# Performance work log

Measured on AMD Instinct MI355X. Metric: run time of the kernel, lower is better.

Reference implementation:

```python
import jax, jax.numpy as jnp
import numpy as np

BN_EPS = 1e-5

def setup_inputs() -> dict:
    key = jax.random.key(0)
    ks = jax.random.split(key, 8)
    B, C, O, M, K, NR, NT = 64, 8, 8, 32, 32, 8, 8
    ini = float(np.sqrt(3.0 / O / C))
    def p(k):
        return jax.random.uniform(k, (O, C), jnp.float32, -ini, ini)
    return {
        "A": jax.random.normal(ks[0], (B, C, M, K, NR, NT), jnp.float32),
        "P1": p(ks[1]), "P2": p(ks[2]), "P3": p(ks[3]), "P4": p(ks[4]), "P5": p(ks[5]),
        "Wq": p(ks[6]), "Wk": p(ks[7]),
        "gamma": jnp.ones((O,), jnp.float32),
        "beta": jnp.zeros((O,), jnp.float32),
    }

def reference(A, P1, P2, P3, P4, P5, Wq, Wk, gamma, beta):
    B, C, M, Kd, NR, NT = A.shape
    # Branch 1: per-element channel mix, full tensor
    A1 = jnp.einsum('oc,bcmkrt->bomkrt', P1, A)                    # [B,O,M,K,NR,NT]
    # Branch 2: mean over M (axis 2)
    A2 = jnp.einsum('oc,bckrt->bokrt', P2, A.mean(2))[:, :, None]  # [B,O,1,K,NR,NT]
    # Branch 3: mean over NT (axis 5)
    A3 = jnp.einsum('oc,bcmkr->bomkr', P3, A.mean(5))[..., None]   # [B,O,M,K,NR,1]
    # Branch 4: mean over NR (axis 4)
    A4 = jnp.einsum('oc,bcmkt->bomkt', P4, A.mean(4))[:, :, :, :, None, :]  # [B,O,M,K,1,NT]
    # Attention branch over the K axis, built from mean over NR
    temp = A.mean(4)                                               # [B,C,M,K,NT]
    q = jnp.einsum('oc,bcmkt->bomkt', Wq, temp)
    k = jnp.einsum('oc,bcmkt->bomkt', Wk, temp)
    v = jnp.einsum('oc,bcmkt->bomkt', P5, temp)
    alpha = jnp.tanh(jnp.einsum('bomkt,bomlt->bomkl', q, k) / NT)  # [B,O,M,K,K]
    A5 = (jnp.einsum('bomkl,bomlt->bomkt', alpha, v) / Kd)[:, :, :, :, None, :]
    out = A1 + 0.1 * A2 + 0.1 * A3 + 0.5 * A4 + 2.0 * A5          # [B,O,M,K,NR,NT]
    out = jax.nn.relu(out)
    # BatchNorm1d (training mode, biased var) over all dims except channel O
    mean = out.mean(axis=(0, 2, 3, 4, 5), keepdims=True)
    var = out.var(axis=(0, 2, 3, 4, 5), keepdims=True)
    g = gamma[None, :, None, None, None, None]
    bta = beta[None, :, None, None, None, None]
    return (out - mean) * jax.lax.rsqrt(var + BN_EPS) * g + bta
```

## Files before the change

kernel.cpp:

```cpp
#include <hip/hip_runtime.h>
#include <hip/hip_fp16.h>


using u16 = unsigned short;
using u32 = unsigned int;
typedef float f32x4 __attribute__((ext_vector_type(4)));

#define NTOT 33554432u
#define PLANE 65536u

__device__ __forceinline__ void ld8f(const float* p, float* f) {
  float4 a = *(const float4*)p;
  float4 b = *(const float4*)(p + 4);
  f[0] = a.x; f[1] = a.y; f[2] = a.z; f[3] = a.w;
  f[4] = b.x; f[5] = b.y; f[6] = b.z; f[7] = b.w;
}
__device__ __forceinline__ void st8f(float* p, const float* f) {
  *(float4*)p = make_float4(f[0], f[1], f[2], f[3]);
  *(float4*)(p + 4) = make_float4(f[4], f[5], f[6], f[7]);
}
__device__ __forceinline__ void st8f_nt(float* p, const float* f) {
  f32x4 a = {f[0], f[1], f[2], f[3]};
  f32x4 b = {f[4], f[5], f[6], f[7]};
  __builtin_nontemporal_store(a, (f32x4*)p);
  __builtin_nontemporal_store(b, (f32x4*)(p + 4));
}
__device__ __forceinline__ u16 f2h(float f) {
  __half h = __float2half_rn(f);
  return *(u16*)&h;
}
__device__ __forceinline__ float h2f(u16 x) {
  __half h = *(__half*)&x;
  return __half2float(h);
}
__device__ __forceinline__ float fast_tanh(float x) {
  float e = __expf(2.0f * x);
  return 1.0f - 2.0f / (e + 1.0f);
}

__global__ __launch_bounds__(1024) void k1a_mmean(
    const float* __restrict__ A, float* __restrict__ mcab,
    float* __restrict__ stats) {
  __shared__ float red[4][256][9];
  const int b = blockIdx.x >> 3;
  const int c = blockIdx.x & 7;
  const int tid = threadIdx.x;
  if (blockIdx.x == 0 && tid < 16) stats[tid] = 0.0f;
  const int mh = tid >> 8;
  const int jt = tid & 255;
  const float* base = A + (size_t)(b * 8 + c) * 65536 + (size_t)mh * 8 * 2048 + jt * 8;
  float acc[8];
#pragma unroll
  for (int t = 0; t < 8; ++t) acc[t] = 0.0f;
#pragma unroll
  for (int m = 0; m < 8; ++m) {
    float ar[8];
    ld8f(base + m * 2048, ar);
#pragma unroll
    for (int t = 0; t < 8; ++t) acc[t] += ar[t];
  }
#pragma unroll
  for (int t = 0; t < 8; ++t) red[mh][jt][t] = acc[t];
  __syncthreads();
  if (mh == 0) {
    float s[8];
#pragma unroll
    for (int t = 0; t < 8; ++t)
      s[t] = (red[0][jt][t] + red[1][jt][t] + red[2][jt][t] + red[3][jt][t]) *
             (1.0f / 32.0f);
    st8f(mcab + (size_t)(b * 8 + c) * 2048 + jt * 8, s);
  }
}

__global__ void k1b_p2(float* __restrict__ mcab, const float* __restrict__ P2) {
  const int b = blockIdx.x >> 3;
  const int j = (blockIdx.x & 7) * 256 + threadIdx.x;
  float mc[8];
#pragma unroll
  for (int c = 0; c < 8; ++c) mc[c] = mcab[(size_t)(b * 8 + c) * 2048 + j];
  float a2[8];
#pragma unroll
  for (int o = 0; o < 8; ++o) {
    float s = 0.0f;
#pragma unroll
    for (int c = 0; c < 8; ++c) s = fmaf(P2[o * 8 + c], mc[c], s);
    a2[o] = 0.1f * s;
  }
#pragma unroll
  for (int o = 0; o < 8; ++o) mcab[(size_t)(b * 8 + o) * 2048 + j] = a2[o];
}

template <int MODE>
__global__ __launch_bounds__(256, 2) void k2_main(
    const float* __restrict__ A,
    const float* __restrict__ a2pre,
    const float* __restrict__ P1,
    const float* __restrict__ P3,
    const float* __restrict__ P4,
    const float* __restrict__ P5,
    const float* __restrict__ Wq,
    const float* __restrict__ Wk,
    float* __restrict__ outp,
    u16* __restrict__ xb,
    float* __restrict__ stats,
    const u32 rsplit) {
  __shared__ float qb[8 * 260];
  __shared__ float kb[8 * 260];
  __shared__ float vb[8 * 260];
  __shared__ float a5b[8 * 260];
  __shared__ float sred[64];

  const int tid = threadIdx.x;
  const int b = blockIdx.x >> 5;
  const int m = blockIdx.x & 31;
  const int k = tid >> 3;
  const int r = tid & 7;

  float acc[8][8];
  float acc3[8];
  float qv[8], kv[8], vv[8];
#pragma unroll
  for (int o = 0; o < 8; ++o) {
    acc3[o] = 0.0f;
#pragma unroll
    for (int t = 0; t < 8; ++t) acc[o][t] = 0.0f;
  }
#pragma unroll
  for (int t = 0; t < 8; ++t) { qv[t] = 0.0f; kv[t] = 0.0f; vv[t] = 0.0f; }

#pragma unroll
  for (int c = 0; c < 8; ++c) {
    float ar[8];
    ld8f(A + ((size_t)((b * 8 + c) * 32 + m) * 2048 + tid * 8), ar);
    float trc[8];
#pragma unroll
    for (int t = 0; t < 8; ++t) {
      float x = ar[t];
      x += __shfl_xor(x, 1, 64);
      x += __shfl_xor(x, 2, 64);
      x += __shfl_xor(x, 4, 64);
      trc[t] = x * 0.125f;
    }
    const float mtc = (ar[0] + ar[1] + ar[2] + ar[3] +
                       ar[4] + ar[5] + ar[6] + ar[7]) * 0.125f;
#pragma unroll
    for (int o = 0; o < 8; ++o) {
      const float w1 = P1[o * 8 + c];
      const float w4 = 0.5f * P4[o * 8 + c];
      acc3[o] = fmaf(0.1f * P3[o * 8 + c], mtc, acc3[o]);
#pragma unroll
      for (int t = 0; t < 8; ++t)
        acc[o][t] = fmaf(w1, ar[t], fmaf(w4, trc[t], acc[o][t]));
    }
    const float wq = Wq[r * 8 + c];
    const float wk = Wk[r * 8 + c];
    const float wv = P5[r * 8 + c];
#pragma unroll
    for (int t = 0; t < 8; ++t) {
      qv[t] = fmaf(wq, trc[t], qv[t]);
      kv[t] = fmaf(wk, trc[t], kv[t]);
      vv[t] = fmaf(wv, trc[t], vv[t]);
    }
  }

#pragma unroll
  for (int o = 0; o < 8; ++o) {
    float a2v[8];
    ld8f(a2pre + ((size_t)(b * 8 + o) * 2048 + tid * 8), a2v);
#pragma unroll
    for (int t = 0; t < 8; ++t) acc[o][t] += a2v[t] + acc3[o];
  }

  st8f(&qb[r * 260 + k * 8], qv);
  st8f(&kb[r * 260 + k * 8], kv);
  st8f(&vb[r * 260 + k * 8], vv);
  __syncthreads();

  {
    const int o = tid >> 5;
    const int kq = (tid >> 2) & 7;
    const int lo = tid & 3;
    float qf[4][8];
#pragma unroll
    for (int kl = 0; kl < 4; ++kl)
      ld8f(&qb[o * 260 + (kq * 4 + kl) * 8], qf[kl]);
    float a5p[4][8];
#pragma unroll
    for (int kl = 0; kl < 4; ++kl)
#pragma unroll
      for (int t = 0; t < 8; ++t) a5p[kl][t] = 0.0f;

#pragma unroll
    for (int ll = 0; ll < 8; ++ll) {
      const int l = lo * 8 + ll;
      float krw[8];
      ld8f(&kb[o * 260 + l * 8], krw);
      float al[4];
#pragma unroll
      for (int kl = 0; kl < 4; ++kl) {
        float s = 0.0f;
#pragma unroll
        for (int t = 0; t < 8; ++t) s = fmaf(qf[kl][t], krw[t], s);
        al[kl] = fast_tanh(s * 0.125f);
      }
      float vrw[8];
      ld8f(&vb[o * 260 + l * 8], vrw);
#pragma unroll
      for (int kl = 0; kl < 4; ++kl)
#pragma unroll
        for (int t = 0; t < 8; ++t)
          a5p[kl][t] = fmaf(al[kl], vrw[t], a5p[kl][t]);
    }
#pragma unroll
    for (int kl = 0; kl < 4; ++kl)
#pragma unroll
      for (int t = 0; t < 8; ++t) {
        float x = a5p[kl][t];
        x += __shfl_xor(x, 1, 64);
        x += __shfl_xor(x, 2, 64);
        a5p[kl][t] = x * 0.0625f;
      }
#pragma unroll
    for (int kl = 0; kl < 4; ++kl) {
      const float w0 = lo == 0 ? a5p[kl][0] : lo == 1 ? a5p[kl][2]
                      : lo == 2 ? a5p[kl][4] : a5p[kl][6];
      const float w1 = lo == 0 ? a5p[kl][1] : lo == 1 ? a5p[kl][3]
                      : lo == 2 ? a5p[kl][5] : a5p[kl][7];
      *(float2*)&a5b[o * 260 + (kq * 4 + kl) * 8 + lo * 2] = make_float2(w0, w1);
    }
  }
  __syncthreads();

  float psum[8], psq[8];
#pragma unroll
  for (int o = 0; o < 8; ++o) { psum[o] = 0.0f; psq[o] = 0.0f; }
  const size_t outbase = (size_t)(b * 256 + m) * 2048 + tid * 8;
#pragma unroll
  for (int o = 0; o < 8; ++o) {
    float a5f[8];
    ld8f(&a5b[o * 260 + k * 8], a5f);
    float x8[8];
#pragma unroll
    for (int t = 0; t < 8; ++t) {
      float x = acc[o][t] + a5f[t];
      x = fmaxf(x, 0.0f);
      psum[o] += x;
      psq[o] = fmaf(x, x, psq[o]);
      x8[t] = x;
    }
    const size_t idx = outbase + (size_t)o * 65536;
    if (MODE == 0) {
      st8f(outp + idx, x8);
    } else {
      uint4 u;
      u.x = (u32)f2h(x8[0]) | ((u32)f2h(x8[1]) << 16);
      u.y = (u32)f2h(x8[2]) | ((u32)f2h(x8[3]) << 16);
      u.z = (u32)f2h(x8[4]) | ((u32)f2h(x8[5]) << 16);
      u.w = (u32)f2h(x8[6]) | ((u32)f2h(x8[7]) << 16);
      u16* dst;
      if (MODE == 1) {
        dst = xb;
      } else {
        dst = (idx >= (size_t)rsplit) ? (u16*)outp : xb;
      }
      *(uint4*)(dst + idx) = u;
    }
  }
#pragma unroll
  for (int o = 0; o < 8; ++o) {
    float s = psum[o], q = psq[o];
#pragma unroll
    for (int mask = 32; mask >= 1; mask >>= 1) {
      s += __shfl_xor(s, mask, 64);
      q += __shfl_xor(q, mask, 64);
    }
    psum[o] = s; psq[o] = q;
  }
  const int lane = tid & 63;
  const int wid = tid >> 6;
  if (lane == 0) {
#pragma unroll
    for (int o = 0; o < 8; ++o) {
      sred[wid * 16 + o * 2] = psum[o];
      sred[wid * 16 + o * 2 + 1] = psq[o];
    }
  }
  __syncthreads();
  if (tid < 16) {
    float s = sred[tid] + sred[16 + tid] + sred[32 + tid] + sred[48 + tid];
    atomicAdd(&stats[tid], s);
  }
}

__global__ void k3_fp16(const u16* __restrict__ src, float* __restrict__ outp,
                        const float* __restrict__ stats,
                        const float* __restrict__ gamma,
                        const float* __restrict__ beta,
                        const u32 ebase) {
  const size_t e0 = (size_t)ebase + ((size_t)blockIdx.x * 256 + threadIdx.x) * 8;
  const int o = (int)(e0 >> 16) & 7;
  const float inv_n = 1.0f / 4194304.0f;
  const float mean = stats[o * 2] * inv_n;
  float var = stats[o * 2 + 1] * inv_n - mean * mean;
  var = fmaxf(var, 0.0f);
  const float inv = rsqrtf(var + 1e-5f);
  const float g = gamma[o] * inv;
  const float sh = beta[o] - mean * g;
  const uint4 u = *(const uint4*)(src + e0);
  float f[8];
  f[0] = h2f((u16)(u.x & 0xffffu)); f[1] = h2f((u16)(u.x >> 16));
  f[2] = h2f((u16)(u.y & 0xffffu)); f[3] = h2f((u16)(u.y >> 16));
  f[4] = h2f((u16)(u.z & 0xffffu)); f[5] = h2f((u16)(u.z >> 16));
  f[6] = h2f((u16)(u.w & 0xffffu)); f[7] = h2f((u16)(u.w >> 16));
#pragma unroll
  for (int t = 0; t < 8; ++t) f[t] = fmaf(f[t], g, sh);
  st8f_nt(outp + e0, f);
}

__global__ void k3_norm_inplace(float* __restrict__ outp,
                                const float* __restrict__ stats,
                                const float* __restrict__ gamma,
                                const float* __restrict__ beta) {
  const int idx = blockIdx.x * 256 + threadIdx.x;
  const size_t e0 = (size_t)idx * 8;
  const int o = (int)(e0 >> 16) & 7;
  const float inv_n = 1.0f / 4194304.0f;
  const float mean = stats[o * 2] * inv_n;
  float var = stats[o * 2 + 1] * inv_n - mean * mean;
  var = fmaxf(var, 0.0f);
  const float inv = rsqrtf(var + 1e-5f);
  const float g = gamma[o] * inv;
  const float sh = beta[o] - mean * g;
  float f[8];
  ld8f(outp + e0, f);
#pragma unroll
  for (int t = 0; t < 8; ++t) f[t] = fmaf(f[t], g, sh);
  st8f_nt(outp + e0, f);
}

extern "C" void kernel_launch(void* const* d_in, const int* in_sizes, int n_in,
                              void* d_out, int out_size, void* d_ws, size_t ws_size,
                              hipStream_t stream) {
  const float* A  = (const float*)d_in[0];
  const float* P1 = (const float*)d_in[1];
  const float* P2 = (const float*)d_in[2];
  const float* P3 = (const float*)d_in[3];
  const float* P4 = (const float*)d_in[4];
  const float* P5 = (const float*)d_in[5];
  const float* Wq = (const float*)d_in[6];
  const float* Wk = (const float*)d_in[7];
  const float* gamma = (const float*)d_in[8];
  const float* beta  = (const float*)d_in[9];
  float* outp = (float*)d_out;

  float* stats = (float*)d_ws;
  float* mcab = (float*)((char*)d_ws + 256);
  u16* xb = (u16*)((char*)d_ws + 256 + (size_t)4 * 1024 * 1024);
  const size_t UWB = 256 + (size_t)4 * 1024 * 1024;
  const size_t need_full = UWB + (size_t)2 * NTOT;

  hipLaunchKernelGGL(k1a_mmean, dim3(512), dim3(1024), 0, stream, A, mcab, stats);
  hipLaunchKernelGGL(k1b_p2, dim3(512), dim3(256), 0, stream, mcab, P2);

  if (ws_size >= need_full) {
    hipLaunchKernelGGL((k2_main<1>), dim3(2048), dim3(256), 0, stream,
                       A, mcab, P1, P3, P4, P5, Wq, Wk, outp, xb, stats, 0u);
    hipLaunchKernelGGL(k3_fp16, dim3(16384), dim3(256), 0, stream,
                       xb, outp, stats, gamma, beta, 0u);
  } else {
    const size_t avail = (ws_size > UWB) ? (ws_size - UWB) : 0;
    u32 R = NTOT / 2;
    while (R > PLANE && (size_t)2 * R > avail) R >>= 1;
    if ((size_t)2 * R <= avail) {
      hipLaunchKernelGGL((k2_main<2>), dim3(2048), dim3(256), 0, stream,
                         A, mcab, P1, P3, P4, P5, Wq, Wk, outp, xb, stats, R);
      for (u32 S = NTOT / 2; S >= R; S >>= 1) {
        hipLaunchKernelGGL(k3_fp16, dim3(S / 2048), dim3(256), 0, stream,
                           (const u16*)outp, outp, stats, gamma, beta, S);
      }
      hipLaunchKernelGGL(k3_fp16, dim3(R / 2048), dim3(256), 0, stream,
                         xb, outp, stats, gamma, beta, 0u);
    } else {
      hipLaunchKernelGGL((k2_main<0>), dim3(2048), dim3(256), 0, stream,
                         A, mcab, P1, P3, P4, P5, Wq, Wk, outp, xb, stats, 0u);
      hipLaunchKernelGGL(k3_norm_inplace, dim3(16384), dim3(256), 0, stream,
                         outp, stats, gamma, beta);
    }
  }
}
```

Measured before the change: 387.3 us.

## Fuse main pass and batchnorm apply via cooperative grid sync with register staging

Replaces the two-pass main kernel plus fp16 workspace normalize kernel with a single cooperative kernel of 512 blocks. Each block processes four m slices, keeps the ReLU outputs packed as fp16 in registers, grid-syncs once the BN statistics are accumulated, then normalizes and writes fp32 output directly. This removes the fp16 intermediate write and read-back through global memory and one kernel launch. In exchange it adds heavy register pressure from the 128-register staging array, a grid-wide barrier, and a fallback path if cooperative launch fails.

```diff
diff --git a/kernel.cpp b/kernel.cpp
--- a/kernel.cpp
+++ b/kernel.cpp
@@ -1,13 +1,13 @@
 #include <hip/hip_runtime.h>
 #include <hip/hip_fp16.h>
+#include <hip/hip_cooperative_groups.h>
+
+namespace cg = cooperative_groups;
 
 
 using u16 = unsigned short;
 using u32 = unsigned int;
 typedef float f32x4 __attribute__((ext_vector_type(4)));
-
-#define NTOT 33554432u
-#define PLANE 65536u
 
 __device__ __forceinline__ void ld8f(const float* p, float* f) {
   float4 a = *(const float4*)p;
@@ -90,7 +90,236 @@
   for (int o = 0; o < 8; ++o) mcab[(size_t)(b * 8 + o) * 2048 + j] = a2[o];
 }
 
-template <int MODE>
+__global__ __launch_bounds__(256, 2) void k2_fused(
+    const float* __restrict__ A,
+    const float* __restrict__ a2pre,
+    const float* __restrict__ P1,
+    const float* __restrict__ P3,
+    const float* __restrict__ P4,
+    const float* __restrict__ P5,
+    const float* __restrict__ Wq,
+    const float* __restrict__ Wk,
+    const float* __restrict__ gamma,
+    const float* __restrict__ beta,
+    float* __restrict__ outp,
+    float* __restrict__ stats) {
+  __shared__ float qb[8 * 260];
+  __shared__ float kb[8 * 260];
+  __shared__ float vb[8 * 260];
+  __shared__ float a5b[8 * 260];
+  __shared__ float sred[64];
+
+  const int tid = threadIdx.x;
+  const int b = blockIdx.x >> 3;
+  const int mg = blockIdx.x & 7;
+  const int k = tid >> 3;
+  const int r = tid & 7;
+
+  u32 stg[4][8][4];
+  float psum[8], psq[8];
+#pragma unroll
+  for (int o = 0; o < 8; ++o) { psum[o] = 0.0f; psq[o] = 0.0f; }
+
+#pragma unroll
+  for (int mi = 0; mi < 4; ++mi) {
+    const int m = mg * 4 + mi;
+
+    float acc[8][8];
+    float acc3[8];
+    float qv[8], kv[8], vv[8];
+#pragma unroll
+    for (int o = 0; o < 8; ++o) {
+      acc3[o] = 0.0f;
+#pragma unroll
+      for (int t = 0; t < 8; ++t) acc[o][t] = 0.0f;
+    }
+#pragma unroll
+    for (int t = 0; t < 8; ++t) { qv[t] = 0.0f; kv[t] = 0.0f; vv[t] = 0.0f; }
+
+#pragma unroll
+    for (int c = 0; c < 8; ++c) {
+      float ar[8];
+      ld8f(A + ((size_t)((b * 8 + c) * 32 + m) * 2048 + tid * 8), ar);
+      float trc[8];
+#pragma unroll
+      for (int t = 0; t < 8; ++t) {
+        float x = ar[t];
+        x += __shfl_xor(x, 1, 64);
+        x += __shfl_xor(x, 2, 64);
+        x += __shfl_xor(x, 4, 64);
+        trc[t] = x * 0.125f;
+      }
+      const float mtc = (ar[0] + ar[1] + ar[2] + ar[3] +
+                         ar[4] + ar[5] + ar[6] + ar[7]) * 0.125f;
+#pragma unroll
+      for (int o = 0; o < 8; ++o) {
+        const float w1 = P1[o * 8 + c];
+        const float w4 = 0.5f * P4[o * 8 + c];
+        acc3[o] = fmaf(0.1f * P3[o * 8 + c], mtc, acc3[o]);
+#pragma unroll
+        for (int t = 0; t < 8; ++t)
+          acc[o][t] = fmaf(w1, ar[t], fmaf(w4, trc[t], acc[o][t]));
+      }
+      const float wq = Wq[r * 8 + c];
+      const float wk = Wk[r * 8 + c];
+      const float wv = P5[r * 8 + c];
+#pragma unroll
+      for (int t = 0; t < 8; ++t) {
+        qv[t] = fmaf(wq, trc[t], qv[t]);
+        kv[t] = fmaf(wk, trc[t], kv[t]);
+        vv[t] = fmaf(wv, trc[t], vv[t]);
+      }
+    }
+
+#pragma unroll
+    for (int o = 0; o < 8; ++o) {
+      float a2v[8];
+      ld8f(a2pre + ((size_t)(b * 8 + o) * 2048 + tid * 8), a2v);
+#pragma unroll
+      for (int t = 0; t < 8; ++t) acc[o][t] += a2v[t] + acc3[o];
+    }
+
+    st8f(&qb[r * 260 + k * 8], qv);
+    st8f(&kb[r * 260 + k * 8], kv);
+    st8f(&vb[r * 260 + k * 8], vv);
+    __syncthreads();
+
+    {
+      const int o = tid >> 5;
+      const int kq = (tid >> 2) & 7;
+      const int lo = tid & 3;
+      float qf[4][8];
+#pragma unroll
+      for (int kl = 0; kl < 4; ++kl)
+        ld8f(&qb[o * 260 + (kq * 4 + kl) * 8], qf[kl]);
+      float a5p[4][8];
+#pragma unroll
+      for (int kl = 0; kl < 4; ++kl)
+#pragma unroll
+        for (int t = 0; t < 8; ++t) a5p[kl][t] = 0.0f;
+
+#pragma unroll
+      for (int ll = 0; ll < 8; ++ll) {
+        const int l = lo * 8 + ll;
+        float krw[8];
+        ld8f(&kb[o * 260 + l * 8], krw);
+        float al[4];
+#pragma unroll
+        for (int kl = 0; kl < 4; ++kl) {
+          float s = 0.0f;
+#pragma unroll
+          for (int t = 0; t < 8; ++t) s = fmaf(qf[kl][t], krw[t], s);
+          al[kl] = fast_tanh(s * 0.125f);
+        }
+        float vrw[8];
+        ld8f(&vb[o * 260 + l * 8], vrw);
+#pragma unroll
+        for (int kl = 0; kl < 4; ++kl)
+#pragma unroll
+          for (int t = 0; t < 8; ++t)
+            a5p[kl][t] = fmaf(al[kl], vrw[t], a5p[kl][t]);
+      }
+#pragma unroll
+      for (int kl = 0; kl < 4; ++kl)
+#pragma unroll
+        for (int t = 0; t < 8; ++t) {
+          float x = a5p[kl][t];
+          x += __shfl_xor(x, 1, 64);
+          x += __shfl_xor(x, 2, 64);
+          a5p[kl][t] = x * 0.0625f;
+        }
+#pragma unroll
+      for (int kl = 0; kl < 4; ++kl) {
+        const float w0 = lo == 0 ? a5p[kl][0] : lo == 1 ? a5p[kl][2]
+                        : lo == 2 ? a5p[kl][4] : a5p[kl][6];
+        const float w1 = lo == 0 ? a5p[kl][1] : lo == 1 ? a5p[kl][3]
+                        : lo == 2 ? a5p[kl][5] : a5p[kl][7];
+        *(float2*)&a5b[o * 260 + (kq * 4 + kl) * 8 + lo * 2] = make_float2(w0, w1);
+      }
+    }
+    __syncthreads();
+
+#pragma unroll
+    for (int o = 0; o < 8; ++o) {
+      float a5f[8];
+      ld8f(&a5b[o * 260 + k * 8], a5f);
+      float x8[8];
+#pragma unroll
+      for (int t = 0; t < 8; ++t) {
+        float x = acc[o][t] + a5f[t];
+        x = fmaxf(x, 0.0f);
+        psum[o] += x;
+        psq[o] = fmaf(x, x, psq[o]);
+        x8[t] = x;
+      }
+      stg[mi][o][0] = (u32)f2h(x8[0]) | ((u32)f2h(x8[1]) << 16);
+      stg[mi][o][1] = (u32)f2h(x8[2]) | ((u32)f2h(x8[3]) << 16);
+      stg[mi][o][2] = (u32)f2h(x8[4]) | ((u32)f2h(x8[5]) << 16);
+      stg[mi][o][3] = (u32)f2h(x8[6]) | ((u32)f2h(x8[7]) << 16);
+    }
+  }
+
+#pragma unroll
+  for (int o = 0; o < 8; ++o) {
+    float s = psum[o], q = psq[o];
+#pragma unroll
+    for (int mask = 32; mask >= 1; mask >>= 1) {
+      s += __shfl_xor(s, mask, 64);
+      q += __shfl_xor(q, mask, 64);
+    }
+    psum[o] = s; psq[o] = q;
+  }
+  const int lane = tid & 63;
+  const int wid = tid >> 6;
+  if (lane == 0) {
+#pragma unroll
+    for (int o = 0; o < 8; ++o) {
+      sred[wid * 16 + o * 2] = psum[o];
+      sred[wid * 16 + o * 2 + 1] = psq[o];
+    }
+  }
+  __syncthreads();
+  if (tid < 16) {
+    float s = sred[tid] + sred[16 + tid] + sred[32 + tid] + sred[48 + tid];
+    atomicAdd(&stats[tid], s);
+  }
+
+  __threadfence();
+  cg::this_grid().sync();
+  __threadfence();
+
+  float gg[8], shh[8];
+#pragma unroll
+  for (int o = 0; o < 8; ++o) {
+    const float inv_n = 1.0f / 4194304.0f;
+    const float mean = stats[o * 2] * inv_n;
+    float var = stats[o * 2 + 1] * inv_n - mean * mean;
+    var = fmaxf(var, 0.0f);
+    const float inv = rsqrtf(var + 1e-5f);
+    gg[o] = gamma[o] * inv;
+    shh[o] = beta[o] - mean * gg[o];
+  }
+#pragma unroll
+  for (int mi = 0; mi < 4; ++mi) {
+    const int m = mg * 4 + mi;
+#pragma unroll
+    for (int o = 0; o < 8; ++o) {
+      float f[8];
+      f[0] = h2f((u16)(stg[mi][o][0] & 0xffffu));
+      f[1] = h2f((u16)(stg[mi][o][0] >> 16));
+      f[2] = h2f((u16)(stg[mi][o][1] & 0xffffu));
+      f[3] = h2f((u16)(stg[mi][o][1] >> 16));
+      f[4] = h2f((u16)(stg[mi][o][2] & 0xffffu));
+      f[5] = h2f((u16)(stg[mi][o][2] >> 16));
+      f[6] = h2f((u16)(stg[mi][o][3] & 0xffffu));
+      f[7] = h2f((u16)(stg[mi][o][3] >> 16));
+#pragma unroll
+      for (int t = 0; t < 8; ++t) f[t] = fmaf(f[t], gg[o], shh[o]);
+      st8f_nt(outp + ((size_t)((b * 8 + o) * 32 + m) * 2048 + tid * 8), f);
+    }
+  }
+}
+
 __global__ __launch_bounds__(256, 2) void k2_main(
     const float* __restrict__ A,
     const float* __restrict__ a2pre,
@@ -101,9 +330,7 @@
     const float* __restrict__ Wq,
     const float* __restrict__ Wk,
     float* __restrict__ outp,
-    u16* __restrict__ xb,
-    float* __restrict__ stats,
-    const u32 rsplit) {
+    float* __restrict__ stats) {
   __shared__ float qb[8 * 260];
   __shared__ float kb[8 * 260];
   __shared__ float vb[8 * 260];
@@ -248,23 +475,7 @@
       psq[o] = fmaf(x, x, psq[o]);
       x8[t] = x;
     }
-    const size_t idx = outbase + (size_t)o * 65536;
-    if (MODE == 0) {
-      st8f(outp + idx, x8);
-    } else {
-      uint4 u;
-      u.x = (u32)f2h(x8[0]) | ((u32)f2h(x8[1]) << 16);
-      u.y = (u32)f2h(x8[2]) | ((u32)f2h(x8[3]) << 16);
-      u.z = (u32)f2h(x8[4]) | ((u32)f2h(x8[5]) << 16);
-      u.w = (u32)f2h(x8[6]) | ((u32)f2h(x8[7]) << 16);
-      u16* dst;
-      if (MODE == 1) {
-        dst = xb;
-      } else {
-        dst = (idx >= (size_t)rsplit) ? (u16*)outp : xb;
-      }
-      *(uint4*)(dst + idx) = u;
-    }
+    st8f(outp + (outbase + (size_t)o * 65536), x8);
   }
 #pragma unroll
   for (int o = 0; o < 8; ++o) {
@@ -290,31 +501,6 @@
     float s = sred[tid] + sred[16 + tid] + sred[32 + tid] + sred[48 + tid];
     atomicAdd(&stats[tid], s);
   }
-}
-
-__global__ void k3_fp16(const u16* __restrict__ src, float* __restrict__ outp,
-                        const float* __restrict__ stats,
-                        const float* __restrict__ gamma,
-                        const float* __restrict__ beta,
-                        const u32 ebase) {
-  const size_t e0 = (size_t)ebase + ((size_t)blockIdx.x * 256 + threadIdx.x) * 8;
-  const int o = (int)(e0 >> 16) & 7;
-  const float inv_n = 1.0f / 4194304.0f;
-  const float mean = stats[o * 2] * inv_n;
-  float var = stats[o * 2 + 1] * inv_n - mean * mean;
-  var = fmaxf(var, 0.0f);
-  const float inv = rsqrtf(var + 1e-5f);
-  const float g = gamma[o] * inv;
-  const float sh = beta[o] - mean * g;
-  const uint4 u = *(const uint4*)(src + e0);
-  float f[8];
-  f[0] = h2f((u16)(u.x & 0xffffu)); f[1] = h2f((u16)(u.x >> 16));
-  f[2] = h2f((u16)(u.y & 0xffffu)); f[3] = h2f((u16)(u.y >> 16));
-  f[4] = h2f((u16)(u.z & 0xffffu)); f[5] = h2f((u16)(u.z >> 16));
-  f[6] = h2f((u16)(u.w & 0xffffu)); f[7] = h2f((u16)(u.w >> 16));
-#pragma unroll
-  for (int t = 0; t < 8; ++t) f[t] = fmaf(f[t], g, sh);
-  st8f_nt(outp + e0, f);
 }
 
 __global__ void k3_norm_inplace(float* __restrict__ outp,
@@ -355,36 +541,22 @@
 
   float* stats = (float*)d_ws;
   float* mcab = (float*)((char*)d_ws + 256);
-  u16* xb = (u16*)((char*)d_ws + 256 + (size_t)4 * 1024 * 1024);
-  const size_t UWB = 256 + (size_t)4 * 1024 * 1024;
-  const size_t need_full = UWB + (size_t)2 * NTOT;
 
   hipLaunchKernelGGL(k1a_mmean, dim3(512), dim3(1024), 0, stream, A, mcab, stats);
   hipLaunchKernelGGL(k1b_p2, dim3(512), dim3(256), 0, stream, mcab, P2);
 
-  if (ws_size >= need_full) {
-    hipLaunchKernelGGL((k2_main<1>), dim3(2048), dim3(256), 0, stream,
-                       A, mcab, P1, P3, P4, P5, Wq, Wk, outp, xb, stats, 0u);
-    hipLaunchKernelGGL(k3_fp16, dim3(16384), dim3(256), 0, stream,
-                       xb, outp, stats, gamma, beta, 0u);
-  } else {
-    const size_t avail = (ws_size > UWB) ? (ws_size - UWB) : 0;
-    u32 R = NTOT / 2;
-    while (R > PLANE && (size_t)2 * R > avail) R >>= 1;
-    if ((size_t)2 * R <= avail) {
-      hipLaunchKernelGGL((k2_main<2>), dim3(2048), dim3(256), 0, stream,
-                         A, mcab, P1, P3, P4, P5, Wq, Wk, outp, xb, stats, R);
-      for (u32 S = NTOT / 2; S >= R; S >>= 1) {
-        hipLaunchKernelGGL(k3_fp16, dim3(S / 2048), dim3(256), 0, stream,
-                           (const u16*)outp, outp, stats, gamma, beta, S);
-      }
-      hipLaunchKernelGGL(k3_fp16, dim3(R / 2048), dim3(256), 0, stream,
-                         xb, outp, stats, gamma, beta, 0u);
-    } else {
-      hipLaunchKernelGGL((k2_main<0>), dim3(2048), dim3(256), 0, stream,
-                         A, mcab, P1, P3, P4, P5, Wq, Wk, outp, xb, stats, 0u);
-      hipLaunchKernelGGL(k3_norm_inplace, dim3(16384), dim3(256), 0, stream,
-                         outp, stats, gamma, beta);
-    }
-  }
-}
+  void* kargs[] = {
+    (void*)&A, (void*)&mcab, (void*)&P1, (void*)&P3, (void*)&P4, (void*)&P5,
+    (void*)&Wq, (void*)&Wk, (void*)&gamma, (void*)&beta, (void*)&outp,
+    (void*)&stats
+  };
+  hipError_t err = hipLaunchCooperativeKernel(
+      (const void*)k2_fused, dim3(512), dim3(256), kargs, 0, stream);
+  if (err != hipSuccess) {
+    (void)hipGetLastError();
+    hipLaunchKernelGGL(k2_main, dim3(2048), dim3(256), 0, stream,
+                       A, mcab, P1, P3, P4, P5, Wq, Wk, outp, stats);
+    hipLaunchKernelGGL(k3_norm_inplace, dim3(16384), dim3(256), 0, stream,
+                       outp, stats, gamma, beta);
+  }
+}
```

Measured after the change: 711.0 us. +83.6%, slower.

## Stage fp16 intermediate in output buffer and expand it in place by slices

Applied to the files above, without the earlier changes.

The main kernel now always writes the fp16 pre-normalisation values into the first half of the output buffer, instead of into a separate workspace region. The lowest 1 MB of those values is copied aside into the workspace. A cascade of slice kernels then expands the upper halves to normalised fp32 in place, working from the top down, and the last slice reads from the saved copy. The q and a5 shared buffers are also merged to cut LDS use, at the cost of an extra barrier. The aim is to drop the large workspace buffer and keep fp16 data in the output lines. In exchange the schedule adds several serialised launches, the smaller of which underfill the GPU.

```diff
diff --git a/kernel.cpp b/kernel.cpp
--- a/kernel.cpp
+++ b/kernel.cpp
@@ -7,7 +7,6 @@
 typedef float f32x4 __attribute__((ext_vector_type(4)));
 
 #define NTOT 33554432u
-#define PLANE 65536u
 
 __device__ __forceinline__ void ld8f(const float* p, float* f) {
   float4 a = *(const float4*)p;
@@ -90,7 +89,6 @@
   for (int o = 0; o < 8; ++o) mcab[(size_t)(b * 8 + o) * 2048 + j] = a2[o];
 }
 
-template <int MODE>
 __global__ __launch_bounds__(256, 2) void k2_main(
     const float* __restrict__ A,
     const float* __restrict__ a2pre,
@@ -101,13 +99,10 @@
     const float* __restrict__ Wq,
     const float* __restrict__ Wk,
     float* __restrict__ outp,
-    u16* __restrict__ xb,
-    float* __restrict__ stats,
-    const u32 rsplit) {
-  __shared__ float qb[8 * 260];
+    float* __restrict__ stats) {
+  __shared__ float qa5[8 * 260];
   __shared__ float kb[8 * 260];
   __shared__ float vb[8 * 260];
-  __shared__ float a5b[8 * 260];
   __shared__ float sred[64];
 
   const int tid = threadIdx.x;
@@ -171,7 +166,7 @@
     for (int t = 0; t < 8; ++t) acc[o][t] += a2v[t] + acc3[o];
   }
 
-  st8f(&qb[r * 260 + k * 8], qv);
+  st8f(&qa5[r * 260 + k * 8], qv);
   st8f(&kb[r * 260 + k * 8], kv);
   st8f(&vb[r * 260 + k * 8], vv);
   __syncthreads();
@@ -183,7 +178,9 @@
     float qf[4][8];
 #pragma unroll
     for (int kl = 0; kl < 4; ++kl)
-      ld8f(&qb[o * 260 + (kq * 4 + kl) * 8], qf[kl]);
+      ld8f(&qa5[o * 260 + (kq * 4 + kl) * 8], qf[kl]);
+    __syncthreads();
+
     float a5p[4][8];
 #pragma unroll
     for (int kl = 0; kl < 4; ++kl)
@@ -226,7 +223,7 @@
                       : lo == 2 ? a5p[kl][4] : a5p[kl][6];
       const float w1 = lo == 0 ? a5p[kl][1] : lo == 1 ? a5p[kl][3]
                       : lo == 2 ? a5p[kl][5] : a5p[kl][7];
-      *(float2*)&a5b[o * 260 + (kq * 4 + kl) * 8 + lo * 2] = make_float2(w0, w1);
+      *(float2*)&qa5[o * 260 + (kq * 4 + kl) * 8 + lo * 2] = make_float2(w0, w1);
     }
   }
   __syncthreads();
@@ -234,11 +231,10 @@
   float psum[8], psq[8];
 #pragma unroll
   for (int o = 0; o < 8; ++o) { psum[o] = 0.0f; psq[o] = 0.0f; }
-  const size_t outbase = (size_t)(b * 256 + m) * 2048 + tid * 8;
 #pragma unroll
   for (int o = 0; o < 8; ++o) {
     float a5f[8];
-    ld8f(&a5b[o * 260 + k * 8], a5f);
+    ld8f(&qa5[o * 260 + k * 8], a5f);
     float x8[8];
 #pragma unroll
     for (int t = 0; t < 8; ++t) {
@@ -248,23 +244,13 @@
       psq[o] = fmaf(x, x, psq[o]);
       x8[t] = x;
     }
-    const size_t idx = outbase + (size_t)o * 65536;
-    if (MODE == 0) {
-      st8f(outp + idx, x8);
-    } else {
-      uint4 u;
-      u.x = (u32)f2h(x8[0]) | ((u32)f2h(x8[1]) << 16);
-      u.y = (u32)f2h(x8[2]) | ((u32)f2h(x8[3]) << 16);
-      u.z = (u32)f2h(x8[4]) | ((u32)f2h(x8[5]) << 16);
-      u.w = (u32)f2h(x8[6]) | ((u32)f2h(x8[7]) << 16);
-      u16* dst;
-      if (MODE == 1) {
-        dst = xb;
-      } else {
-        dst = (idx >= (size_t)rsplit) ? (u16*)outp : xb;
-      }
-      *(uint4*)(dst + idx) = u;
-    }
+    uint4 u;
+    u.x = (u32)f2h(x8[0]) | ((u32)f2h(x8[1]) << 16);
+    u.y = (u32)f2h(x8[2]) | ((u32)f2h(x8[3]) << 16);
+    u.z = (u32)f2h(x8[4]) | ((u32)f2h(x8[5]) << 16);
+    u.w = (u32)f2h(x8[6]) | ((u32)f2h(x8[7]) << 16);
+    const size_t e = (size_t)((b * 8 + o) * 32 + m) * 2048 + tid * 8;
+    *(uint4*)((char*)outp + 2 * e) = u;
   }
 #pragma unroll
   for (int o = 0; o < 8; ++o) {
@@ -292,11 +278,16 @@
   }
 }
 
-__global__ void k3_fp16(const u16* __restrict__ src, float* __restrict__ outp,
-                        const float* __restrict__ stats,
-                        const float* __restrict__ gamma,
-                        const float* __restrict__ beta,
-                        const u32 ebase) {
+__global__ void k3_copy(const uint4* __restrict__ src, uint4* __restrict__ dst) {
+  const int i = blockIdx.x * 256 + threadIdx.x;
+  dst[i] = src[i];
+}
+
+__global__ void k3_slice(const u16* __restrict__ src, float* __restrict__ outp,
+                         const float* __restrict__ stats,
+                         const float* __restrict__ gamma,
+                         const float* __restrict__ beta,
+                         const u32 ebase) {
   const size_t e0 = (size_t)ebase + ((size_t)blockIdx.x * 256 + threadIdx.x) * 8;
   const int o = (int)(e0 >> 16) & 7;
   const float inv_n = 1.0f / 4194304.0f;
@@ -317,27 +308,6 @@
   st8f_nt(outp + e0, f);
 }
 
-__global__ void k3_norm_inplace(float* __restrict__ outp,
-                                const float* __restrict__ stats,
-                                const float* __restrict__ gamma,
-                                const float* __restrict__ beta) {
-  const int idx = blockIdx.x * 256 + threadIdx.x;
-  const size_t e0 = (size_t)idx * 8;
-  const int o = (int)(e0 >> 16) & 7;
-  const float inv_n = 1.0f / 4194304.0f;
-  const float mean = stats[o * 2] * inv_n;
-  float var = stats[o * 2 + 1] * inv_n - mean * mean;
-  var = fmaxf(var, 0.0f);
-  const float inv = rsqrtf(var + 1e-5f);
-  const float g = gamma[o] * inv;
-  const float sh = beta[o] - mean * g;
-  float f[8];
-  ld8f(outp + e0, f);
-#pragma unroll
-  for (int t = 0; t < 8; ++t) f[t] = fmaf(f[t], g, sh);
-  st8f_nt(outp + e0, f);
-}
-
 extern "C" void kernel_launch(void* const* d_in, const int* in_sizes, int n_in,
                               void* d_out, int out_size, void* d_ws, size_t ws_size,
                               hipStream_t stream) {
@@ -355,36 +325,20 @@
 
   float* stats = (float*)d_ws;
   float* mcab = (float*)((char*)d_ws + 256);
-  u16* xb = (u16*)((char*)d_ws + 256 + (size_t)4 * 1024 * 1024);
-  const size_t UWB = 256 + (size_t)4 * 1024 * 1024;
-  const size_t need_full = UWB + (size_t)2 * NTOT;
 
   hipLaunchKernelGGL(k1a_mmean, dim3(512), dim3(1024), 0, stream, A, mcab, stats);
   hipLaunchKernelGGL(k1b_p2, dim3(512), dim3(256), 0, stream, mcab, P2);
-
-  if (ws_size >= need_full) {
-    hipLaunchKernelGGL((k2_main<1>), dim3(2048), dim3(256), 0, stream,
-                       A, mcab, P1, P3, P4, P5, Wq, Wk, outp, xb, stats, 0u);
-    hipLaunchKernelGGL(k3_fp16, dim3(16384), dim3(256), 0, stream,
-                       xb, outp, stats, gamma, beta, 0u);
-  } else {
-    const size_t avail = (ws_size > UWB) ? (ws_size - UWB) : 0;
-    u32 R = NTOT / 2;
-    while (R > PLANE && (size_t)2 * R > avail) R >>= 1;
-    if ((size_t)2 * R <= avail) {
-      hipLaunchKernelGGL((k2_main<2>), dim3(2048), dim3(256), 0, stream,
-                         A, mcab, P1, P3, P4, P5, Wq, Wk, outp, xb, stats, R);
-      for (u32 S = NTOT / 2; S >= R; S >>= 1) {
-        hipLaunchKernelGGL(k3_fp16, dim3(S / 2048), dim3(256), 0, stream,
-                           (const u16*)outp, outp, stats, gamma, beta, S);
-      }
-      hipLaunchKernelGGL(k3_fp16, dim3(R / 2048), dim3(256), 0, stream,
-                         xb, outp, stats, gamma, beta, 0u);
-    } else {
-      hipLaunchKernelGGL((k2_main<0>), dim3(2048), dim3(256), 0, stream,
-                         A, mcab, P1, P3, P4, P5, Wq, Wk, outp, xb, stats, 0u);
-      hipLaunchKernelGGL(k3_norm_inplace, dim3(16384), dim3(256), 0, stream,
-                         outp, stats, gamma, beta);
-    }
-  }
-}
+  hipLaunchKernelGGL(k2_main, dim3(2048), dim3(256), 0, stream,
+                     A, mcab, P1, P3, P4, P5, Wq, Wk, outp, stats);
+
+  hipLaunchKernelGGL(k3_copy, dim3(256), dim3(256), 0, stream,
+                     (const uint4*)outp, (uint4*)mcab);
+
+  const u16* s16 = (const u16*)outp;
+  for (u32 n = NTOT / 2; n >= 524288u; n >>= 1) {
+    hipLaunchKernelGGL(k3_slice, dim3(n / 2048), dim3(256), 0, stream,
+                       s16, outp, stats, gamma, beta, n);
+  }
+  hipLaunchKernelGGL(k3_slice, dim3(256), dim3(256), 0, stream,
+                     (const u16*)mcab, outp, stats, gamma, beta, 0u);
+}
```

Measured after the change: 397.4 us. 2.6% more time.
